# Performance work log

Measured on AMD Instinct MI355X. Metric: run time of the kernel, lower is better.

## Reference

```python
import jax, jax.numpy as jnp
import numpy as np

N_NODES = 100000
N_EDGES = 1600000
D = 128
BETA = 0.001
EPS = 1e-12  # F.normalize eps


def setup_inputs() -> dict:
    key = jax.random.key(0)
    k1, k2, k3, k4, k5, k6 = jax.random.split(key, 6)
    stdv = 1.0 / np.sqrt(D)
    return {
        "input": jax.random.normal(k1, (N_NODES, D), dtype=jnp.float32),
        "edge_rows": jax.random.randint(k2, (N_EDGES,), 0, N_NODES, dtype=jnp.int32),
        "edge_cols": jax.random.randint(k3, (N_EDGES,), 0, N_NODES, dtype=jnp.int32),
        "edge_vals": jax.random.uniform(k4, (N_EDGES,), dtype=jnp.float32),
        "weight": jax.random.uniform(k5, (D, D), minval=-stdv, maxval=stdv, dtype=jnp.float32),
        "bias": jax.random.uniform(k6, (D,), minval=-stdv, maxval=stdv, dtype=jnp.float32),
    }


def reference(input, edge_rows, edge_cols, edge_vals, weight, bias):
    # dense projection: [N, D]
    support = input @ weight
    # sparse neighbor aggregation: agg[i] = sum_{(i,j) in E} adj_val * support[j]
    msgs = edge_vals[:, None] * support[edge_cols]          # [E, D]
    agg = jax.ops.segment_sum(msgs, edge_rows, num_segments=input.shape[0])
    # beta-weighted residual blend
    out = BETA * input + (1.0 - BETA) * agg
    # row-wise L2 normalize (torch F.normalize, p=2, dim=1)
    norm = jnp.sqrt(jnp.sum(out * out, axis=1, keepdims=True))
    out = out / jnp.maximum(norm, EPS)
    # bias add
    return out + bias
```

## Files before the change

### kernel.cpp

```cpp
#include <hip/hip_runtime.h>

#define N_NODES 100000
#define N_EDGES 1600000
#define D 128
#define NB 1563
#define NSUB 8
#define SUBCAP 224
#define CAP (NSUB*SUBCAP)

typedef short bf16x8 __attribute__((ext_vector_type(8)));
typedef float f32x4 __attribute__((ext_vector_type(4)));

__device__ __forceinline__ unsigned short f2bf(float x){
  union { float f; unsigned u; } v; v.f = x;
  unsigned r = v.u + 0x7fffu + ((v.u >> 16) & 1u);
  return (unsigned short)(r >> 16);
}

__device__ __forceinline__ float bf2f(unsigned short h){
  union { unsigned u; float f; } v; v.u = ((unsigned)h) << 16;
  return v.f;
}

__global__ __launch_bounds__(256) void convert_input(const float4* __restrict__ in4,
                                                     ushort4* __restrict__ outb,
                                                     const float* __restrict__ W,
                                                     unsigned short* __restrict__ WT){
  int i = blockIdx.x*256 + threadIdx.x;
  if (i < D*D){
    int k = i >> 7, c = i & 127;
    WT[c*128 + k] = f2bf(W[i]);
  }
  float4 a = in4[i];
  ushort4 h;
  h.x = f2bf(a.x); h.y = f2bf(a.y); h.z = f2bf(a.z); h.w = f2bf(a.w);
  outb[i] = h;
}

__global__ __launch_bounds__(256) void scatter_direct(const int* __restrict__ rows,
                                                      const int* __restrict__ cols,
                                                      const float* __restrict__ vals,
                                                      int* __restrict__ cursor,
                                                      int2* __restrict__ edges_s){
  int i = blockIdx.x*256 + threadIdx.x;
  int s = blockIdx.x & (NSUB-1);
  int r = rows[i];
  int b = r >> 6;
  int pos = atomicAdd(&cursor[s*NB + b], 1);
  if (pos < SUBCAP)
    edges_s[(size_t)b*CAP + s*SUBCAP + pos] =
        make_int2(cols[i] | ((r & 63) << 17), __float_as_int(vals[i]));
}

__global__ __launch_bounds__(512) void agg_final(const ushort4* __restrict__ inb4,
                                                 const int* __restrict__ cursor,
                                                 const int2* __restrict__ edges_g,
                                                 const unsigned short* __restrict__ WTg,
                                                 const float* __restrict__ bias,
                                                 float* __restrict__ out){
  __shared__ unsigned short As[64*136];
  __shared__ int hist[64];
  __shared__ int cur[64];
  __shared__ int rs[64];
  __shared__ int rc[64];
  __shared__ float rsum[2][64];
  int2* st = (int2*)As;

  int t = threadIdx.x;
  int b = blockIdx.x;
  size_t base = (size_t)b * CAP;

  if (t < 64) hist[t] = 0;
  __syncthreads();

  int2 held[NSUB];
  int hv = 0;
  #pragma unroll
  for (int s = 0; s < NSUB; ++s){
    int ms = cursor[s*NB + b];
    if (ms > SUBCAP) ms = SUBCAP;
    if (t < ms){
      int2 e = edges_g[base + s*SUBCAP + t];
      held[s] = e;
      hv |= (1 << s);
      atomicAdd(&hist[((unsigned)e.x) >> 17], 1);
    }
  }
  __syncthreads();

  if (t < 64){
    int c = hist[t];
    int x = c;
    #pragma unroll
    for (int o = 1; o < 64; o <<= 1){
      int y = __shfl_up(x, o);
      if (t >= o) x += y;
    }
    int excl = x - c;
    cur[t] = excl;
    rs[t] = excl;
    rc[t] = c;
  }
  __syncthreads();

  #pragma unroll
  for (int s = 0; s < NSUB; ++s){
    if (hv & (1 << s)){
      int2 e = held[s];
      int r = ((unsigned)e.x) >> 17;
      int pos = atomicAdd(&cur[r], 1);
      st[pos] = make_int2(e.x & 0x1FFFF, e.y);
    }
  }
  __syncthreads();

  int grp = t >> 5, l = t & 31;
  float4 res[4];
  #pragma unroll
  for (int j = 0; j < 4; ++j){
    int r = grp*4 + j;
    int e = rs[r], end = e + rc[r];
    float4 a0 = make_float4(0.f,0.f,0.f,0.f);
    float4 a1 = make_float4(0.f,0.f,0.f,0.f);
    float4 a2 = make_float4(0.f,0.f,0.f,0.f);
    float4 a3 = make_float4(0.f,0.f,0.f,0.f);
    for (; e + 4 <= end; e += 4){
      int2 e0 = st[e+0];
      int2 e1 = st[e+1];
      int2 e2 = st[e+2];
      int2 e3 = st[e+3];
      ushort4 x0 = inb4[(size_t)e0.x*32 + l];
      ushort4 x1 = inb4[(size_t)e1.x*32 + l];
      ushort4 x2 = inb4[(size_t)e2.x*32 + l];
      ushort4 x3 = inb4[(size_t)e3.x*32 + l];
      float v0 = __int_as_float(e0.y), v1 = __int_as_float(e1.y);
      float v2 = __int_as_float(e2.y), v3 = __int_as_float(e3.y);
      a0.x = fmaf(v0, bf2f(x0.x), a0.x); a0.y = fmaf(v0, bf2f(x0.y), a0.y);
      a0.z = fmaf(v0, bf2f(x0.z), a0.z); a0.w = fmaf(v0, bf2f(x0.w), a0.w);
      a1.x = fmaf(v1, bf2f(x1.x), a1.x); a1.y = fmaf(v1, bf2f(x1.y), a1.y);
      a1.z = fmaf(v1, bf2f(x1.z), a1.z); a1.w = fmaf(v1, bf2f(x1.w), a1.w);
      a2.x = fmaf(v2, bf2f(x2.x), a2.x); a2.y = fmaf(v2, bf2f(x2.y), a2.y);
      a2.z = fmaf(v2, bf2f(x2.z), a2.z); a2.w = fmaf(v2, bf2f(x2.w), a2.w);
      a3.x = fmaf(v3, bf2f(x3.x), a3.x); a3.y = fmaf(v3, bf2f(x3.y), a3.y);
      a3.z = fmaf(v3, bf2f(x3.z), a3.z); a3.w = fmaf(v3, bf2f(x3.w), a3.w);
    }
    for (; e < end; ++e){
      int2 ee = st[e];
      ushort4 x = inb4[(size_t)ee.x*32 + l];
      float v = __int_as_float(ee.y);
      a0.x = fmaf(v, bf2f(x.x), a0.x); a0.y = fmaf(v, bf2f(x.y), a0.y);
      a0.z = fmaf(v, bf2f(x.z), a0.z); a0.w = fmaf(v, bf2f(x.w), a0.w);
    }
    res[j].x = (a0.x + a1.x) + (a2.x + a3.x);
    res[j].y = (a0.y + a1.y) + (a2.y + a3.y);
    res[j].z = (a0.z + a1.z) + (a2.z + a3.z);
    res[j].w = (a0.w + a1.w) + (a2.w + a3.w);
  }
  __syncthreads();

  #pragma unroll
  for (int j = 0; j < 4; ++j){
    int r = grp*4 + j;
    ushort4 h;
    h.x = f2bf(res[j].x); h.y = f2bf(res[j].y);
    h.z = f2bf(res[j].z); h.w = f2bf(res[j].w);
    *((ushort4*)&As[r*136 + l*4]) = h;
  }
  __syncthreads();

  int w = t >> 6, lane = t & 63;
  int wr = w >> 1, wc = w & 1;
  int q = lane >> 4, n = lane & 15;
  bf16x8 afr[4];
  #pragma unroll
  for (int ks = 0; ks < 4; ++ks)
    afr[ks] = *((const bf16x8*)&As[(wr*16 + n)*136 + ks*32 + q*8]);
  __syncthreads();

  int block_row = b * 64;
  #pragma unroll
  for (int i = 0; i < 4; ++i){
    int idx4 = i*512 + t;
    int row = idx4 >> 5, k4 = idx4 & 31;
    int grow = block_row + row;
    ushort4 h = make_ushort4(0,0,0,0);
    if (grow < N_NODES) h = inb4[(size_t)grow*32 + k4];
    *((ushort4*)&As[row*136 + k4*4]) = h;
  }
  __syncthreads();

  f32x4 acc[4];
  #pragma unroll
  for (int ct = 0; ct < 4; ++ct) acc[ct] = (f32x4){0.f, 0.f, 0.f, 0.f};

  #pragma unroll
  for (int ct = 0; ct < 4; ++ct){
    #pragma unroll
    for (int ks = 0; ks < 4; ++ks){
      bf16x8 bfr = *((const bf16x8*)(WTg + (wc*64 + ct*16 + n)*128 + ks*32 + q*8));
      acc[ct] = __builtin_amdgcn_mfma_f32_16x16x32_bf16(afr[ks], bfr, acc[ct], 0, 0, 0);
    }
  }

  float v[4][4];
  float s[4] = {0.f, 0.f, 0.f, 0.f};
  #pragma unroll
  for (int reg = 0; reg < 4; ++reg){
    int row_local = wr*16 + q*4 + reg;
    #pragma unroll
    for (int ct = 0; ct < 4; ++ct){
      float inp = bf2f(As[row_local*136 + wc*64 + ct*16 + n]);
      float val = fmaf(0.999f, acc[ct][reg], 0.001f * inp);
      v[ct][reg] = val;
      s[reg] = fmaf(val, val, s[reg]);
    }
  }
  #pragma unroll
  for (int reg = 0; reg < 4; ++reg){
    float x = s[reg];
    x += __shfl_xor(x, 1);
    x += __shfl_xor(x, 2);
    x += __shfl_xor(x, 4);
    x += __shfl_xor(x, 8);
    s[reg] = x;
  }
  if (n == 0){
    #pragma unroll
    for (int reg = 0; reg < 4; ++reg)
      rsum[wc][wr*16 + q*4 + reg] = s[reg];
  }
  __syncthreads();

  #pragma unroll
  for (int reg = 0; reg < 4; ++reg){
    int row_local = wr*16 + q*4 + reg;
    int grow = block_row + row_local;
    if (grow >= N_NODES) continue;
    float tot = rsum[0][row_local] + rsum[1][row_local];
    float scale = 1.f / fmaxf(sqrtf(tot), 1e-12f);
    float* outrow = out + (size_t)grow * D;
    #pragma unroll
    for (int ct = 0; ct < 4; ++ct){
      int c = wc*64 + ct*16 + n;
      outrow[c] = fmaf(v[ct][reg], scale, bias[c]);
    }
  }
}

extern "C" void kernel_launch(void* const* d_in, const int* in_sizes, int n_in,
                              void* d_out, int out_size, void* d_ws, size_t ws_size,
                              hipStream_t stream){
  const float* input  = (const float*)d_in[0];
  const int*   erows  = (const int*)d_in[1];
  const int*   ecols  = (const int*)d_in[2];
  const float* evals  = (const float*)d_in[3];
  const float* weight = (const float*)d_in[4];
  const float* bias   = (const float*)d_in[5];
  float* out = (float*)d_out;

  int*   cursor    = (int*)d_ws;
  int2*  edges_s   = (int2*)(cursor + NSUB*NB);
  ushort4* inb     = (ushort4*)(edges_s + (size_t)NB*CAP);
  unsigned short* WTg = (unsigned short*)(inb + (size_t)N_NODES * 32);

  hipMemsetAsync(cursor, 0, (size_t)NSUB * NB * sizeof(int), stream);
  convert_input<<<12500, 256, 0, stream>>>((const float4*)input, inb, weight, WTg);
  scatter_direct<<<N_EDGES/256, 256, 0, stream>>>(erows, ecols, evals, cursor, edges_s);
  agg_final<<<NB, 512, 0, stream>>>((const ushort4*)inb, cursor, edges_s,
                                    WTg, bias, out);
}
```

Baseline: 322.2 us.

## Balance row gather with atomic work queue, separate LDS buffers, fold memset into convert

After: 306.5 us. -4.9%, faster.

```diff
diff --git a/kernel.cpp b/kernel.cpp
--- a/kernel.cpp
+++ b/kernel.cpp
@@ -24,9 +24,11 @@
 
 __global__ __launch_bounds__(256) void convert_input(const float4* __restrict__ in4,
                                                      ushort4* __restrict__ outb,
+                                                     int* __restrict__ cursor,
                                                      const float* __restrict__ W,
                                                      unsigned short* __restrict__ WT){
   int i = blockIdx.x*256 + threadIdx.x;
+  if (i < NSUB*NB) cursor[i] = 0;
   if (i < D*D){
     int k = i >> 7, c = i & 127;
     WT[c*128 + k] = f2bf(W[i]);
@@ -58,19 +60,23 @@
                                                  const unsigned short* __restrict__ WTg,
                                                  const float* __restrict__ bias,
                                                  float* __restrict__ out){
+  __shared__ __align__(16) unsigned char pool[64*136*2];
   __shared__ unsigned short As[64*136];
   __shared__ int hist[64];
   __shared__ int cur[64];
   __shared__ int rs[64];
   __shared__ int rc[64];
   __shared__ float rsum[2][64];
-  int2* st = (int2*)As;
+  __shared__ int rowctr;
+  int2* st = (int2*)pool;
+  unsigned short* Bs = (unsigned short*)pool;
 
   int t = threadIdx.x;
   int b = blockIdx.x;
   size_t base = (size_t)b * CAP;
 
   if (t < 64) hist[t] = 0;
+  if (t == 0) rowctr = 0;
   __syncthreads();
 
   int2 held[NSUB];
@@ -114,11 +120,13 @@
   }
   __syncthreads();
 
-  int grp = t >> 5, l = t & 31;
-  float4 res[4];
-  #pragma unroll
-  for (int j = 0; j < 4; ++j){
-    int r = grp*4 + j;
+  int l = t & 31;
+  for (;;){
+    int r = 0;
+    if (l == 0) r = atomicAdd(&rowctr, 1);
+    r = __shfl(r, 0, 32);
+    if (r >= 64) break;
+
     int e = rs[r], end = e + rc[r];
     float4 a0 = make_float4(0.f,0.f,0.f,0.f);
     float4 a1 = make_float4(0.f,0.f,0.f,0.f);
@@ -151,19 +159,14 @@
       a0.x = fmaf(v, bf2f(x.x), a0.x); a0.y = fmaf(v, bf2f(x.y), a0.y);
       a0.z = fmaf(v, bf2f(x.z), a0.z); a0.w = fmaf(v, bf2f(x.w), a0.w);
     }
-    res[j].x = (a0.x + a1.x) + (a2.x + a3.x);
-    res[j].y = (a0.y + a1.y) + (a2.y + a3.y);
-    res[j].z = (a0.z + a1.z) + (a2.z + a3.z);
-    res[j].w = (a0.w + a1.w) + (a2.w + a3.w);
-  }
-  __syncthreads();
-
-  #pragma unroll
-  for (int j = 0; j < 4; ++j){
-    int r = grp*4 + j;
+    float4 sres;
+    sres.x = (a0.x + a1.x) + (a2.x + a3.x);
+    sres.y = (a0.y + a1.y) + (a2.y + a3.y);
+    sres.z = (a0.z + a1.z) + (a2.z + a3.z);
+    sres.w = (a0.w + a1.w) + (a2.w + a3.w);
     ushort4 h;
-    h.x = f2bf(res[j].x); h.y = f2bf(res[j].y);
-    h.z = f2bf(res[j].z); h.w = f2bf(res[j].w);
+    h.x = f2bf(sres.x); h.y = f2bf(sres.y);
+    h.z = f2bf(sres.z); h.w = f2bf(sres.w);
     *((ushort4*)&As[r*136 + l*4]) = h;
   }
   __syncthreads();
@@ -171,13 +174,8 @@
   int w = t >> 6, lane = t & 63;
   int wr = w >> 1, wc = w & 1;
   int q = lane >> 4, n = lane & 15;
-  bf16x8 afr[4];
-  #pragma unroll
-  for (int ks = 0; ks < 4; ++ks)
-    afr[ks] = *((const bf16x8*)&As[(wr*16 + n)*136 + ks*32 + q*8]);
-  __syncthreads();
-
   int block_row = b * 64;
+
   #pragma unroll
   for (int i = 0; i < 4; ++i){
     int idx4 = i*512 + t;
@@ -185,14 +183,17 @@
     int grow = block_row + row;
     ushort4 h = make_ushort4(0,0,0,0);
     if (grow < N_NODES) h = inb4[(size_t)grow*32 + k4];
-    *((ushort4*)&As[row*136 + k4*4]) = h;
-  }
-  __syncthreads();
+    *((ushort4*)&Bs[row*136 + k4*4]) = h;
+  }
+
+  bf16x8 afr[4];
+  #pragma unroll
+  for (int ks = 0; ks < 4; ++ks)
+    afr[ks] = *((const bf16x8*)&As[(wr*16 + n)*136 + ks*32 + q*8]);
 
   f32x4 acc[4];
   #pragma unroll
   for (int ct = 0; ct < 4; ++ct) acc[ct] = (f32x4){0.f, 0.f, 0.f, 0.f};
-
   #pragma unroll
   for (int ct = 0; ct < 4; ++ct){
     #pragma unroll
@@ -201,6 +202,7 @@
       acc[ct] = __builtin_amdgcn_mfma_f32_16x16x32_bf16(afr[ks], bfr, acc[ct], 0, 0, 0);
     }
   }
+  __syncthreads();
 
   float v[4][4];
   float s[4] = {0.f, 0.f, 0.f, 0.f};
@@ -209,7 +211,7 @@
     int row_local = wr*16 + q*4 + reg;
     #pragma unroll
     for (int ct = 0; ct < 4; ++ct){
-      float inp = bf2f(As[row_local*136 + wc*64 + ct*16 + n]);
+      float inp = bf2f(Bs[row_local*136 + wc*64 + ct*16 + n]);
       float val = fmaf(0.999f, acc[ct][reg], 0.001f * inp);
       v[ct][reg] = val;
       s[reg] = fmaf(val, val, s[reg]);
@@ -263,8 +265,7 @@
   ushort4* inb     = (ushort4*)(edges_s + (size_t)NB*CAP);
   unsigned short* WTg = (unsigned short*)(inb + (size_t)N_NODES * 32);
 
-  hipMemsetAsync(cursor, 0, (size_t)NSUB * NB * sizeof(int), stream);
-  convert_input<<<12500, 256, 0, stream>>>((const float4*)input, inb, weight, WTg);
+  convert_input<<<12500, 256, 0, stream>>>((const float4*)input, inb, cursor, weight, WTg);
   scatter_direct<<<N_EDGES/256, 256, 0, stream>>>(erows, ecols, evals, cursor, edges_s);
   agg_final<<<NB, 512, 0, stream>>>((const ushort4*)inb, cursor, edges_s,
                                     WTg, bias, out);
```
